# Performance work log

Hardware: AMD Instinct MI355X
Metric: run time of the kernel (lower is better)

Reference implementation:

```python
import jax, jax.numpy as jnp
import numpy as np

TEMPERATURE = 0.07
EPS = 1e-12  # matches torch F.normalize default eps


def setup_inputs() -> dict:
    key = jax.random.key(0)
    k1, k2 = jax.random.split(key)
    B, D = 8192, 256
    anchor = jax.random.normal(k1, (B, D), dtype=jnp.float32)
    positive = jax.random.normal(k2, (B, D), dtype=jnp.float32)
    return {"anchor": anchor, "positive": positive}


def _l2_normalize(x):
    # torch F.normalize(p=2, dim=1): x / max(||x||, eps)
    n = jnp.sqrt(jnp.sum(x * x, axis=1, keepdims=True))
    return x / jnp.maximum(n, EPS)


def reference(anchor, positive):
    a = _l2_normalize(anchor)
    p = _l2_normalize(positive)
    # normalized vectors -> cosine similarity is just a GEMM: (B, B)
    sim = jnp.einsum('id,jd->ij', a, p)
    B = sim.shape[0]
    # hard negative mining: max over off-diagonal entries per row
    neg = jnp.where(jnp.eye(B, dtype=bool), -jnp.inf, sim)
    max_neg = jnp.max(neg, axis=-1)  # (B,)
    logits = jnp.concatenate([sim, max_neg[:, None]], axis=1) / TEMPERATURE  # (B, B+1)
    labels = jnp.arange(B)
    logp = jax.nn.log_softmax(logits, axis=-1)
    loss = -jnp.mean(jnp.take_along_axis(logp, labels[:, None], axis=1))
    return loss
```

## Files before the change

### kernel.cpp

```cpp
#include <hip/hip_runtime.h>
#include <hip/hip_bf16.h>

using floatx4 = __attribute__((ext_vector_type(4))) float;
using int4v   = __attribute__((ext_vector_type(4))) int;
using int8v   = __attribute__((ext_vector_type(8))) int;

#define TEMP_INV 14.285714285714286f
#define DD 256
#define BM 128
#define NCT 4
#define SC1 127

typedef const __attribute__((address_space(1))) unsigned int* gptr_t;
typedef __attribute__((address_space(3))) unsigned int* lptr_t;

__device__ __forceinline__ void async_cp16(const void* g, void* l) {
  __builtin_amdgcn_global_load_lds((gptr_t)g, (lptr_t)l, 16, 0, 0);
}

__global__ __launch_bounds__(256) void nrm_kernel(
    const float* __restrict__ anchor, const float* __restrict__ positive,
    unsigned char* __restrict__ a8, unsigned char* __restrict__ p8,
    float* __restrict__ diag) {
  const int wave = threadIdx.x >> 6;
  const int lane = threadIdx.x & 63;
  const int row  = blockIdx.x * 4 + wave;
  const float4 va = ((const float4*)(anchor   + (size_t)row * DD))[lane];
  const float4 vp = ((const float4*)(positive + (size_t)row * DD))[lane];
  float sa = va.x * va.x + va.y * va.y + va.z * va.z + va.w * va.w;
  float sp = vp.x * vp.x + vp.y * vp.y + vp.z * vp.z + vp.w * vp.w;
#pragma unroll
  for (int m = 32; m >= 1; m >>= 1) {
    sa += __shfl_xor(sa, m, 64);
    sp += __shfl_xor(sp, m, 64);
  }
  const float ka = 1.0f / fmaxf(sqrtf(sa), 1e-12f);
  const float kp = 1.0f / fmaxf(sqrtf(sp), 1e-12f);
  int pa = __builtin_amdgcn_cvt_pk_fp8_f32(va.x * ka, va.y * ka, 0, false);
  pa     = __builtin_amdgcn_cvt_pk_fp8_f32(va.z * ka, va.w * ka, pa, true);
  int pp = __builtin_amdgcn_cvt_pk_fp8_f32(vp.x * kp, vp.y * kp, 0, false);
  pp     = __builtin_amdgcn_cvt_pk_fp8_f32(vp.z * kp, vp.w * kp, pp, true);
  ((int*)(a8 + (size_t)row * DD))[lane] = pa;
  ((int*)(p8 + (size_t)row * DD))[lane] = pp;
  float d = __builtin_amdgcn_cvt_f32_fp8(pa, 0) * __builtin_amdgcn_cvt_f32_fp8(pp, 0)
          + __builtin_amdgcn_cvt_f32_fp8(pa, 1) * __builtin_amdgcn_cvt_f32_fp8(pp, 1)
          + __builtin_amdgcn_cvt_f32_fp8(pa, 2) * __builtin_amdgcn_cvt_f32_fp8(pp, 2)
          + __builtin_amdgcn_cvt_f32_fp8(pa, 3) * __builtin_amdgcn_cvt_f32_fp8(pp, 3);
#pragma unroll
  for (int m = 32; m >= 1; m >>= 1) d += __shfl_xor(d, m, 64);
  if (lane == 0) diag[row] = d;
}

__device__ __forceinline__ int8v bfrag(const unsigned char* Bs, int row, int ks,
                                       int quad, int l16) {
  const int c0 = ks * 8 + quad * 2;
  const int4v lo = *(const int4v*)(Bs + row * DD + (((c0 + 0) ^ l16) << 4));
  const int4v hi = *(const int4v*)(Bs + row * DD + (((c0 + 1) ^ l16) << 4));
  return __builtin_shufflevector(lo, hi, 0, 1, 2, 3, 4, 5, 6, 7);
}

__global__ __launch_bounds__(512, 4) void gemm_stats(
    const unsigned char* __restrict__ a8, const unsigned char* __restrict__ p8,
    float* __restrict__ rsum, float* __restrict__ rmax, int Btot) {
  __shared__ __align__(16) unsigned char Bs[BM * DD];
  __shared__ float red_sum[2][BM];
  __shared__ float red_max[2][BM];

  const int t = threadIdx.x;
  const int wave = t >> 6, lane = t & 63;
  const int wm = wave & 3, wn = wave >> 2;
  const int quad = lane >> 4, l16 = lane & 15;
  const int row0    = blockIdx.y * BM;
  const int colbase = blockIdx.x * (NCT * BM);
  const bool hasdiag = ((int)(blockIdx.y >> 2) == (int)blockIdx.x);

  const int r4   = lane >> 4;
  const int cg   = lane & 15;

  int8v af[2][2];
#pragma unroll
  for (int mi = 0; mi < 2; ++mi)
#pragma unroll
    for (int ks = 0; ks < 2; ++ks)
      af[mi][ks] = *(const int8v*)(a8 +
          (size_t)(row0 + wm * 32 + mi * 16 + l16) * DD + ks * 128 + quad * 32);

#pragma unroll
  for (int q = 0; q < 4; ++q) {
    const int rb = q * 32 + wave * 4;
    const int r  = rb + r4;
    async_cp16(p8 + (size_t)(colbase + r) * DD + (cg ^ (r & 15)) * 16,
               &Bs[rb * DD]);
  }

  float se_run[2][4], mx_run[2][4];
#pragma unroll
  for (int a = 0; a < 2; ++a)
#pragma unroll
    for (int b = 0; b < 4; ++b) { se_run[a][b] = 0.f; mx_run[a][b] = -INFINITY; }

  for (int ct = 0; ct < NCT; ++ct) {
    __syncthreads();

    floatx4 acc[2][4];
#pragma unroll
    for (int a = 0; a < 2; ++a)
#pragma unroll
      for (int b = 0; b < 4; ++b) acc[a][b] = (floatx4){0.f, 0.f, 0.f, 0.f};

#pragma unroll
    for (int ks = 0; ks < 2; ++ks) {
#pragma unroll
      for (int ni = 0; ni < 4; ++ni) {
        const int8v bf = bfrag(Bs, wn * 64 + ni * 16 + l16, ks, quad, l16);
#pragma unroll
        for (int mi = 0; mi < 2; ++mi)
          acc[mi][ni] = __builtin_amdgcn_mfma_scale_f32_16x16x128_f8f6f4(
              af[mi][ks], bf, acc[mi][ni], 0, 0, 0, SC1, 0, SC1);
      }
    }

    __syncthreads();
    if (ct + 1 < NCT) {
      const int colb = colbase + (ct + 1) * BM;
#pragma unroll
      for (int q = 0; q < 4; ++q) {
        const int rb = q * 32 + wave * 4;
        const int r  = rb + r4;
        async_cp16(p8 + (size_t)(colb + r) * DD + (cg ^ (r & 15)) * 16,
                   &Bs[rb * DD]);
      }
    }

    const int col0 = colbase + ct * BM;
    if (!hasdiag) {
#pragma unroll
      for (int mi = 0; mi < 2; ++mi)
#pragma unroll
        for (int reg = 0; reg < 4; ++reg)
#pragma unroll
          for (int ni = 0; ni < 4; ++ni) {
            const float s = acc[mi][ni][reg];
            se_run[mi][reg] += __expf(s * TEMP_INV);
            mx_run[mi][reg] = fmaxf(mx_run[mi][reg], s);
          }
    } else {
#pragma unroll
      for (int mi = 0; mi < 2; ++mi)
#pragma unroll
        for (int reg = 0; reg < 4; ++reg) {
          const int i = row0 + wm * 32 + mi * 16 + quad * 4 + reg;
#pragma unroll
          for (int ni = 0; ni < 4; ++ni) {
            const float s = acc[mi][ni][reg];
            const int j = col0 + wn * 64 + ni * 16 + l16;
            se_run[mi][reg] += __expf(s * TEMP_INV);
            mx_run[mi][reg] = fmaxf(mx_run[mi][reg], (i == j) ? -INFINITY : s);
          }
        }
    }
  }

#pragma unroll
  for (int mi = 0; mi < 2; ++mi) {
#pragma unroll
    for (int reg = 0; reg < 4; ++reg) {
      float se = se_run[mi][reg], mx = mx_run[mi][reg];
#pragma unroll
      for (int m = 1; m < 16; m <<= 1) {
        se += __shfl_xor(se, m, 64);
        mx = fmaxf(mx, __shfl_xor(mx, m, 64));
      }
      if (l16 == 0) {
        const int rb = wm * 32 + mi * 16 + quad * 4 + reg;
        red_sum[wn][rb] = se;
        red_max[wn][rb] = mx;
      }
    }
  }
  __syncthreads();
  if (t < BM) {
    rsum[(size_t)blockIdx.x * Btot + row0 + t] = red_sum[0][t] + red_sum[1][t];
    rmax[(size_t)blockIdx.x * Btot + row0 + t] = fmaxf(red_max[0][t], red_max[1][t]);
  }
}

__global__ __launch_bounds__(256) void row_loss_kernel(
    const float* __restrict__ rsum, const float* __restrict__ rmax,
    const float* __restrict__ diag, float* __restrict__ out, int Btot, int NG) {
  const int i = blockIdx.x * 256 + threadIdx.x;
  float s = 0.f, m = -INFINITY;
  for (int c = 0; c < NG; ++c) {
    s += rsum[(size_t)c * Btot + i];
    m = fmaxf(m, rmax[(size_t)c * Btot + i]);
  }
  float rl = __logf(s + __expf(m * TEMP_INV)) - diag[i] * TEMP_INV;
#pragma unroll
  for (int mm = 32; mm >= 1; mm >>= 1) rl += __shfl_xor(rl, mm, 64);
  __shared__ float red[4];
  if ((threadIdx.x & 63) == 0) red[threadIdx.x >> 6] = rl;
  __syncthreads();
  if (threadIdx.x == 0)
    atomicAdd(out, (red[0] + red[1] + red[2] + red[3]) / (float)Btot);
}

extern "C" void kernel_launch(void* const* d_in, const int* in_sizes, int n_in,
                              void* d_out, int out_size, void* d_ws, size_t ws_size,
                              hipStream_t stream) {
  const float* anchor   = (const float*)d_in[0];
  const float* positive = (const float*)d_in[1];
  const int B  = in_sizes[0] / DD;
  const int NG = B / (BM * NCT);
  const size_t BD = (size_t)B * DD;

  unsigned char* a8 = (unsigned char*)d_ws;
  unsigned char* p8 = a8 + BD;
  float* rsum  = (float*)(p8 + BD);
  float* rmax  = rsum + (size_t)NG * B;
  float* diag  = rmax + (size_t)NG * B;

  (void)hipMemsetAsync(d_out, 0, sizeof(float), stream);
  nrm_kernel<<<B / 4, 256, 0, stream>>>(anchor, positive, a8, p8, diag);
  dim3 g2(NG, B / BM);
  gemm_stats<<<g2, 512, 0, stream>>>(a8, p8, rsum, rmax, B);
  row_loss_kernel<<<B / 256, 256, 0, stream>>>(rsum, rmax, diag, (float*)d_out, B, NG);
}
```

Measured before the change: 118.6 us.

## Stage A tile in LDS asynchronously and fuse final reduction into one block

Anchor fragments are no longer loaded straight from global memory into registers. The A tile is now copied asynchronously into a swizzled LDS buffer alongside the B tile, and fragments are read from LDS per k-step, which cuts register pressure and global load latency. The row-loss kernel becomes a single 1024-thread block that writes the output directly, so the memset and the atomics go away. The cost is 32 KB more LDS per block, which may reduce occupancy from the requested 4 blocks per CU, plus a serial single-block final pass.

```diff
diff --git a/kernel.cpp b/kernel.cpp
--- a/kernel.cpp
+++ b/kernel.cpp
@@ -51,17 +51,18 @@
   if (lane == 0) diag[row] = d;
 }
 
-__device__ __forceinline__ int8v bfrag(const unsigned char* Bs, int row, int ks,
-                                       int quad, int l16) {
+__device__ __forceinline__ int8v frag(const unsigned char* S, int row, int ks,
+                                      int quad, int l16) {
   const int c0 = ks * 8 + quad * 2;
-  const int4v lo = *(const int4v*)(Bs + row * DD + (((c0 + 0) ^ l16) << 4));
-  const int4v hi = *(const int4v*)(Bs + row * DD + (((c0 + 1) ^ l16) << 4));
+  const int4v lo = *(const int4v*)(S + row * DD + (((c0 + 0) ^ l16) << 4));
+  const int4v hi = *(const int4v*)(S + row * DD + (((c0 + 1) ^ l16) << 4));
   return __builtin_shufflevector(lo, hi, 0, 1, 2, 3, 4, 5, 6, 7);
 }
 
 __global__ __launch_bounds__(512, 4) void gemm_stats(
     const unsigned char* __restrict__ a8, const unsigned char* __restrict__ p8,
     float* __restrict__ rsum, float* __restrict__ rmax, int Btot) {
+  __shared__ __align__(16) unsigned char As[BM * DD];
   __shared__ __align__(16) unsigned char Bs[BM * DD];
   __shared__ float red_sum[2][BM];
   __shared__ float red_max[2][BM];
@@ -74,17 +75,16 @@
   const int colbase = blockIdx.x * (NCT * BM);
   const bool hasdiag = ((int)(blockIdx.y >> 2) == (int)blockIdx.x);
 
-  const int r4   = lane >> 4;
-  const int cg   = lane & 15;
-
-  int8v af[2][2];
-#pragma unroll
-  for (int mi = 0; mi < 2; ++mi)
-#pragma unroll
-    for (int ks = 0; ks < 2; ++ks)
-      af[mi][ks] = *(const int8v*)(a8 +
-          (size_t)(row0 + wm * 32 + mi * 16 + l16) * DD + ks * 128 + quad * 32);
-
+  const int r4 = lane >> 4;
+  const int cg = lane & 15;
+
+#pragma unroll
+  for (int q = 0; q < 4; ++q) {
+    const int rb = q * 32 + wave * 4;
+    const int r  = rb + r4;
+    async_cp16(a8 + (size_t)(row0 + r) * DD + (cg ^ (r & 15)) * 16,
+               &As[rb * DD]);
+  }
 #pragma unroll
   for (int q = 0; q < 4; ++q) {
     const int rb = q * 32 + wave * 4;
@@ -110,13 +110,15 @@
 
 #pragma unroll
     for (int ks = 0; ks < 2; ++ks) {
+      const int8v af0 = frag(As, wm * 32 + l16,      ks, quad, l16);
+      const int8v af1 = frag(As, wm * 32 + 16 + l16, ks, quad, l16);
 #pragma unroll
       for (int ni = 0; ni < 4; ++ni) {
-        const int8v bf = bfrag(Bs, wn * 64 + ni * 16 + l16, ks, quad, l16);
-#pragma unroll
-        for (int mi = 0; mi < 2; ++mi)
-          acc[mi][ni] = __builtin_amdgcn_mfma_scale_f32_16x16x128_f8f6f4(
-              af[mi][ks], bf, acc[mi][ni], 0, 0, 0, SC1, 0, SC1);
+        const int8v bf = frag(Bs, wn * 64 + ni * 16 + l16, ks, quad, l16);
+        acc[0][ni] = __builtin_amdgcn_mfma_scale_f32_16x16x128_f8f6f4(
+            af0, bf, acc[0][ni], 0, 0, 0, SC1, 0, SC1);
+        acc[1][ni] = __builtin_amdgcn_mfma_scale_f32_16x16x128_f8f6f4(
+            af1, bf, acc[1][ni], 0, 0, 0, SC1, 0, SC1);
       }
     }
 
@@ -185,23 +187,29 @@
   }
 }
 
-__global__ __launch_bounds__(256) void row_loss_kernel(
+__global__ __launch_bounds__(1024) void row_loss_final(
     const float* __restrict__ rsum, const float* __restrict__ rmax,
     const float* __restrict__ diag, float* __restrict__ out, int Btot, int NG) {
-  const int i = blockIdx.x * 256 + threadIdx.x;
-  float s = 0.f, m = -INFINITY;
-  for (int c = 0; c < NG; ++c) {
-    s += rsum[(size_t)c * Btot + i];
-    m = fmaxf(m, rmax[(size_t)c * Btot + i]);
-  }
-  float rl = __logf(s + __expf(m * TEMP_INV)) - diag[i] * TEMP_INV;
-#pragma unroll
-  for (int mm = 32; mm >= 1; mm >>= 1) rl += __shfl_xor(rl, mm, 64);
-  __shared__ float red[4];
-  if ((threadIdx.x & 63) == 0) red[threadIdx.x >> 6] = rl;
+  float tot = 0.f;
+  for (int i = threadIdx.x; i < Btot; i += 1024) {
+    float s = 0.f, m = -INFINITY;
+    for (int c = 0; c < NG; ++c) {
+      s += rsum[(size_t)c * Btot + i];
+      m = fmaxf(m, rmax[(size_t)c * Btot + i]);
+    }
+    tot += __logf(s + __expf(m * TEMP_INV)) - diag[i] * TEMP_INV;
+  }
+#pragma unroll
+  for (int mm = 32; mm >= 1; mm >>= 1) tot += __shfl_xor(tot, mm, 64);
+  __shared__ float red[16];
+  if ((threadIdx.x & 63) == 0) red[threadIdx.x >> 6] = tot;
   __syncthreads();
-  if (threadIdx.x == 0)
-    atomicAdd(out, (red[0] + red[1] + red[2] + red[3]) / (float)Btot);
+  if (threadIdx.x == 0) {
+    float s = 0.f;
+#pragma unroll
+    for (int w = 0; w < 16; ++w) s += red[w];
+    out[0] = s / (float)Btot;
+  }
 }
 
 extern "C" void kernel_launch(void* const* d_in, const int* in_sizes, int n_in,
@@ -219,9 +227,8 @@
   float* rmax  = rsum + (size_t)NG * B;
   float* diag  = rmax + (size_t)NG * B;
 
-  (void)hipMemsetAsync(d_out, 0, sizeof(float), stream);
   nrm_kernel<<<B / 4, 256, 0, stream>>>(anchor, positive, a8, p8, diag);
   dim3 g2(NG, B / BM);
   gemm_stats<<<g2, 512, 0, stream>>>(a8, p8, rsum, rmax, B);
-  row_loss_kernel<<<B / 256, 256, 0, stream>>>(rsum, rmax, diag, (float*)d_out, B, NG);
-}
+  row_loss_final<<<1, 1024, 0, stream>>>(rsum, rmax, diag, (float*)d_out, B, NG);
+}
```

Measured after the change: 130.4 us. +9.9%, slower.
